# Optimization experiments

Hardware: AMD Instinct MI355X
Metric: run time of the kernel (lower is better)

Reference implementation:

```python
import jax, jax.numpy as jnp
import numpy as np

B, S, H = 32768, 16, 16  # batch, seq_len, G_hiddensize (code requires H == S and H == latent_dim == 16)
LATENT = 16
DISC_DIMS = [(1, 32), (32, 16), (16, 8), (8, 16), (16, 32)]


def setup_inputs() -> dict:
    key = jax.random.key(0)
    ks = iter(jax.random.split(key, 64))
    def p(shape, scale=0.1):
        return (jax.random.normal(next(ks), shape, dtype=jnp.float32) * scale)
    inp = dict(
        values=jax.random.normal(next(ks), (B, S), dtype=jnp.float32),
        masks=jax.random.randint(next(ks), (B, S), 0, 2).astype(jnp.int32),
        g_fwd_Wih=p((4 * H, 1)), g_fwd_Whh=p((4 * H, H)), g_fwd_b=p((4 * H,)),
        g_bwd_Wih=p((4 * H, 1)), g_bwd_Whh=p((4 * H, H)), g_bwd_b=p((4 * H,)),
        imp_W=p((1, H)), imp_b=p((1,)),
        fc_W=p((LATENT, H)), fc_b=p((LATENT,)),
        dec_Wih=p((4 * H, LATENT)), dec_Whh=p((4 * H, H)), dec_b=p((4 * H,)),
        dec_out_W=p((1, H)), dec_out_b=p((1,)),
        disc_out_W=p((1, 32)), disc_out_b=p((1,)),
    )
    for k, (i, h) in enumerate(DISC_DIMS):
        inp[f"d_W_{k}"] = p((4 * h, i))
        inp[f"d_b_{k}"] = p((4 * h,))
    return inp


def lstm_cell(x, h, c, Wih, Whh, b):
    gates = x @ Wih.T + h @ Whh.T + b
    i, f, g, o = jnp.split(gates, 4, axis=-1)
    c = jax.nn.sigmoid(f) * c + jax.nn.sigmoid(i) * jnp.tanh(g)
    h = jax.nn.sigmoid(o) * jnp.tanh(c)
    return h, c


def _forward(values, masks, g_fwd_Wih, g_fwd_Whh, g_fwd_b, g_bwd_Wih, g_bwd_Whh, g_bwd_b,
             imp_W, imp_b, fc_W, fc_b, dec_Wih, dec_Whh, dec_b, dec_out_W, dec_out_b,
             disc_out_W, disc_out_b,
             d_W_0, d_b_0, d_W_1, d_b_1, d_W_2, d_b_2, d_W_3, d_b_3, d_W_4, d_b_4):
    dt = values.dtype
    Bsz = values.shape[0]
    x = values[:, :, None]                     # (B, S, 1)
    m = masks.astype(dt)[:, :, None]           # (B, S, 1)
    # NOTE: torch.flip along axis 2 (size 1) is a no-op, so the bwd cell sees the
    # same (un-reversed) sequence as the fwd cell -- faithfully reproduced here.
    zH = jnp.zeros((Bsz, H), dt)
    h_f, c_f = lstm_cell(jnp.full((Bsz, 1), 128.0, dt), zH, zH, g_fwd_Wih, g_fwd_Whh, g_fwd_b)
    h_b, c_b = lstm_cell(jnp.full((Bsz, 1), -128.0, dt), zH, zH, g_bwd_Wih, g_bwd_Whh, g_bwd_b)

    def gen_step(carry, xm):
        h_f, c_f, h_b, c_b = carry
        x_t, m_t = xm                          # (B,1) each
        cc_f = (1 - m_t) * x_t + m_t * (h_f @ imp_W.T + imp_b)
        cc_b = (1 - m_t) * x_t + m_t * (h_b @ imp_W.T + imp_b)
        h_f, c_f = lstm_cell(cc_f, h_f, c_f, g_fwd_Wih, g_fwd_Whh, g_fwd_b)
        h_b, c_b = lstm_cell(cc_b, h_b, c_b, g_bwd_Wih, g_bwd_Whh, g_bwd_b)
        return (h_f, c_f, h_b, c_b), None

    (h_f, c_f, h_b, c_b), _ = jax.lax.scan(
        gen_step, (h_f, c_f, h_b, c_b),
        (jnp.transpose(x, (1, 0, 2)), jnp.transpose(m, (1, 0, 2))))
    h = h_f + h_b                               # (B, H), H == S
    imputations = h.reshape(Bsz, S, 1)
    imputed = imputations * (1 - m) + x * m      # (B, S, 1)

    # Discriminator: torch calls each LSTMCell WITHOUT state every timestep, so
    # hidden/cell start at zero each call -> purely feedforward per (batch, t).
    # W_hh @ 0 == 0, so only W_ih and the combined bias matter. Vectorize over B*S.
    inp = imputed.reshape(Bsz * S, 1)
    for W, b in ((d_W_0, d_b_0), (d_W_1, d_b_1), (d_W_2, d_b_2), (d_W_3, d_b_3), (d_W_4, d_b_4)):
        gates = inp @ W.T + b
        i, f, g, o = jnp.split(gates, 4, axis=-1)
        cc = jax.nn.sigmoid(i) * jnp.tanh(g)
        inp = jax.nn.sigmoid(o) * jnp.tanh(cc)
    disc_output = (inp @ disc_out_W.T + disc_out_b).reshape(Bsz, S, 1)

    latent = h @ fc_W.T + fc_b                  # (B, 16)

    # Decoder: ignores latent values (only uses batch size); start token = 128s.
    hd = cd = jnp.zeros((Bsz, H), dt)
    hd, cd = lstm_cell(jnp.full((Bsz, LATENT), 128.0, dt), hd, cd, dec_Wih, dec_Whh, dec_b)

    def dec_step(carry, _):
        hd, cd = carry
        hd, cd = lstm_cell(cd, hd, cd, dec_Wih, dec_Whh, dec_b)
        return (hd, cd), hd @ dec_out_W.T + dec_out_b

    _, outs = jax.lax.scan(dec_step, (hd, cd), None, length=S)  # (S, B, 1)
    reconstructed = jnp.transpose(outs, (1, 0, 2))
    return imputed, disc_output, latent, reconstructed


def reference(values, masks, g_fwd_Wih, g_fwd_Whh, g_fwd_b, g_bwd_Wih, g_bwd_Whh, g_bwd_b,
              imp_W, imp_b, fc_W, fc_b, dec_Wih, dec_Whh, dec_b, dec_out_W, dec_out_b,
              disc_out_W, disc_out_b,
              d_W_0, d_b_0, d_W_1, d_b_1, d_W_2, d_b_2, d_W_3, d_b_3, d_W_4, d_b_4):
    return _forward(values, masks, g_fwd_Wih, g_fwd_Whh, g_fwd_b, g_bwd_Wih, g_bwd_Whh, g_bwd_b,
                    imp_W, imp_b, fc_W, fc_b, dec_Wih, dec_Whh, dec_b, dec_out_W, dec_out_b,
                    disc_out_W, disc_out_b,
                    d_W_0, d_b_0, d_W_1, d_b_1, d_W_2, d_b_2, d_W_3, d_b_3, d_W_4, d_b_4)
```

## Files before the change

### kernel.cpp

```cpp
#include <hip/hip_runtime.h>

#define BB 32768
#define BS (BB*16)

typedef __attribute__((ext_vector_type(8))) short bf8v;
typedef __attribute__((ext_vector_type(4))) float f4v;

#define RECO 64
#define TAB  128
#define NTAB 2049
#define HFO  8448
#define HBO  (HFO+BS)

#define PW0 0
#define PB0 96
#define PW1 192
#define PB1 1920
#define PW2 1968
#define PB2 2448
#define PW3 2472
#define PB3 3048
#define PW4 3096
#define PB4 5016
#define POW 5112
#define POB 5144
#define PNU 5148

#define SMF 2580

#define NSCAN 1024
#define NTABB 129

__device__ __forceinline__ float sigm(float x){
    return __builtin_amdgcn_rcpf(1.f + __expf(-x));
}
__device__ __forceinline__ float tanh_f(float x){
    return 1.f - 2.f * __builtin_amdgcn_rcpf(1.f + __expf(2.f * x));
}
__device__ __forceinline__ float dunit(float gi, float gg, float go){
    return sigm(go) * tanh_f(sigm(gi) * tanh_f(gg));
}
__device__ __forceinline__ unsigned short f2bf(float f){
    union { float f; unsigned int i; } v; v.f = f;
    unsigned int x = v.i;
    unsigned int r = x + 0x7fffu + ((x >> 16) & 1u);
    return (unsigned short)(r >> 16);
}
__device__ __forceinline__ float bfu(unsigned short s){
    union { unsigned u; float f; } v; v.u = ((unsigned)s) << 16; return v.f;
}
__device__ __forceinline__ float bflo(unsigned p){
    union { unsigned u; float f; } v; v.u = p << 16; return v.f;
}
__device__ __forceinline__ float bfhi(unsigned p){
    union { unsigned u; float f; } v; v.u = p & 0xffff0000u; return v.f;
}

struct P29 { const float* p[29]; };

__device__ __forceinline__ bf8v makeB(const float* Whh, const float* Wih,
                                      int row, int quad)
{
    bf8v B = {0,0,0,0,0,0,0,0};
    if (quad < 2) {
        const float4* p = (const float4*)(Whh + row*16 + quad*8);
        float4 a0 = p[0], a1 = p[1];
        B[0]=(short)f2bf(a0.x); B[1]=(short)f2bf(a0.y);
        B[2]=(short)f2bf(a0.z); B[3]=(short)f2bf(a0.w);
        B[4]=(short)f2bf(a1.x); B[5]=(short)f2bf(a1.y);
        B[6]=(short)f2bf(a1.z); B[7]=(short)f2bf(a1.w);
    } else if (quad == 2) {
        B[0] = (short)f2bf(Wih[row]);
    }
    return B;
}

__global__ __launch_bounds__(256)
void k_main(P29 a, const int* __restrict__ masks, float* __restrict__ ws)
{
    __shared__ __align__(16) float smem[SMF];
    int tid = threadIdx.x;

    if (blockIdx.x >= NTABB + 1) {
        int lane = tid & 63;
        int wv   = tid >> 6;
        int m    = lane & 15;
        int quad = lane >> 4;
        int sb   = blockIdx.x - (NTABB + 1);
        int dir  = sb >= 512 ? 1 : 0;
        int gid0 = sb * 64 + wv * 16;
        int b0   = gid0 & 32767;

        const float* __restrict__ Wih = a.p[2 + 3*dir];
        const float* __restrict__ Whh = a.p[3 + 3*dir];
        const float* __restrict__ bia = a.p[4 + 3*dir];

        bf8v Ai = makeB(Whh, Wih, m,      quad);
        bf8v Af = makeB(Whh, Wih, 16+m,   quad);
        bf8v Ag = makeB(Whh, Wih, 32+m,   quad);
        bf8v Ao = makeB(Whh, Wih, 48+m,   quad);
        bf8v Ap = {0,0,0,0,0,0,0,0};
        if (quad < 2) {
            const float4* p = (const float4*)(a.p[8] + quad*8);
            float4 a0 = p[0], a1 = p[1];
            Ap[0]=(short)f2bf(a0.x); Ap[1]=(short)f2bf(a0.y);
            Ap[2]=(short)f2bf(a0.z); Ap[3]=(short)f2bf(a0.w);
            Ap[4]=(short)f2bf(a1.x); Ap[5]=(short)f2bf(a1.y);
            Ap[6]=(short)f2bf(a1.z); Ap[7]=(short)f2bf(a1.w);
        }
        float impb = a.p[9][0];
        f4v cimp = {impb, impb, impb, impb};

        f4v cbi, cbf, cbg, cbo;
        {
            float4 t;
            t = *(const float4*)(bia +      quad*4); cbi = (f4v){t.x,t.y,t.z,t.w};
            t = *(const float4*)(bia + 16 + quad*4); cbf = (f4v){t.x,t.y,t.z,t.w};
            t = *(const float4*)(bia + 32 + quad*4); cbg = (f4v){t.x,t.y,t.z,t.w};
            t = *(const float4*)(bia + 48 + quad*4); cbo = (f4v){t.x,t.y,t.z,t.w};
        }

        float sgn = dir ? -128.f : 128.f;
        float c[4], hl[4];
        {
            float4 wI = *(const float4*)(Wih +      quad*4);
            float4 wG = *(const float4*)(Wih + 32 + quad*4);
            float4 wO = *(const float4*)(Wih + 48 + quad*4);
            float wIv[4] = {wI.x, wI.y, wI.z, wI.w};
            float wGv[4] = {wG.x, wG.y, wG.z, wG.w};
            float wOv[4] = {wO.x, wO.y, wO.z, wO.w};
            #pragma unroll
            for (int r = 0; r < 4; r++) {
                float gi0 = sgn*wIv[r] + cbi[r];
                float gg0 = sgn*wGv[r] + cbg[r];
                float go0 = sgn*wOv[r] + cbo[r];
                float c0 = sigm(gi0) * tanh_f(gg0);
                c[r] = c0;
                hl[r] = sigm(go0) * tanh_f(c0);
            }
        }
        unsigned u01, u23;
        asm("v_cvt_pk_bf16_f32 %0, %1, %2" : "=v"(u01) : "v"(hl[0]), "v"(hl[1]));
        asm("v_cvt_pk_bf16_f32 %0, %1, %2" : "=v"(u23) : "v"(hl[2]), "v"(hl[3]));

        int pa0 = ((m + quad*32)      & 63) << 2;
        int pa1 = ((m + quad*32 + 16) & 63) << 2;

        const float* xrow = a.p[0] + (size_t)(b0 + m) * 16;
        const int*   mrow = masks  + (size_t)(b0 + m) * 16;

        #pragma unroll
        for (int t4 = 0; t4 < 4; t4++) {
            float4 x4 = *(const float4*)(xrow + t4*4);
            int4   m4 = *(const int4*)(mrow + t4*4);
            float xa[4] = {x4.x, x4.y, x4.z, x4.w};
            int   ma[4] = {m4.x, m4.y, m4.z, m4.w};
            #pragma unroll
            for (int j = 0; j < 4; j++) {
                union { int i[4]; bf8v v; } B;
                int w0 = __builtin_amdgcn_ds_bpermute(pa0, (int)u01);
                int w1 = __builtin_amdgcn_ds_bpermute(pa0, (int)u23);
                int w2 = __builtin_amdgcn_ds_bpermute(pa1, (int)u01);
                int w3 = __builtin_amdgcn_ds_bpermute(pa1, (int)u23);
                bool hi2 = quad >= 2;
                B.i[0] = hi2 ? 0 : w0;
                B.i[1] = hi2 ? 0 : w1;
                B.i[2] = hi2 ? 0 : w2;
                B.i[3] = hi2 ? 0 : w3;
                f4v dimp = __builtin_amdgcn_mfma_f32_16x16x32_bf16(Ap, B.v, cimp, 0, 0, 0);
                float cc = ma[j] ? dimp[0] : xa[j];
                unsigned ccw;
                asm("v_cvt_pk_bf16_f32 %0, %1, %2" : "=v"(ccw) : "v"(cc), "v"(0.f));
                B.i[0] = (quad == 2) ? (int)ccw : B.i[0];
                f4v di  = __builtin_amdgcn_mfma_f32_16x16x32_bf16(Ai, B.v, cbi, 0, 0, 0);
                f4v df_ = __builtin_amdgcn_mfma_f32_16x16x32_bf16(Af, B.v, cbf, 0, 0, 0);
                f4v dg  = __builtin_amdgcn_mfma_f32_16x16x32_bf16(Ag, B.v, cbg, 0, 0, 0);
                f4v dO  = __builtin_amdgcn_mfma_f32_16x16x32_bf16(Ao, B.v, cbo, 0, 0, 0);
                #pragma unroll
                for (int r = 0; r < 4; r++) {
                    float cn = sigm(df_[r]) * c[r] + sigm(di[r]) * tanh_f(dg[r]);
                    c[r] = cn;
                    hl[r] = sigm(dO[r]) * tanh_f(cn);
                }
                asm("v_cvt_pk_bf16_f32 %0, %1, %2" : "=v"(u01) : "v"(hl[0]), "v"(hl[1]));
                asm("v_cvt_pk_bf16_f32 %0, %1, %2" : "=v"(u23) : "v"(hl[2]), "v"(hl[3]));
            }
        }
        float* outp = ws + HFO + (size_t)dir*BS + (size_t)b0*16;
        #pragma unroll
        for (int r = 0; r < 4; r++) outp[m*16 + quad*4 + r] = hl[r];
        return;
    }

    if (blockIdx.x >= 1) {
        unsigned short* wl = (unsigned short*)smem;
#define STAGE(WS, BSi, h, K, padK, wdst, bdst) \
    { const float* Wp = a.p[WS]; const float* Bp2 = a.p[BSi]; \
      for (int i = tid; i < 3*(h)*(K); i += 256){ \
        int r = i/(K), k = i - r*(K); int g = r/(h), u0 = r - g*(h); \
        int sr = (g==0? u0 : (g==1? 2*(h)+u0 : 3*(h)+u0)); \
        wl[(wdst) + r*(padK) + k] = f2bf(Wp[sr*(K) + k]); } \
      for (int i = tid; i < 3*(h); i += 256){ \
        int g = i/(h), u0 = i - g*(h); \
        int sr = (g==0? u0 : (g==1? 2*(h)+u0 : 3*(h)+u0)); \
        wl[(bdst) + i] = f2bf(Bp2[sr]); } }
        STAGE(19, 20, 32,  1,  1, PW0, PB0)
        STAGE(21, 22, 16, 32, 36, PW1, PB1)
        STAGE(23, 24,  8, 16, 20, PW2, PB2)
        STAGE(25, 26, 16,  8, 12, PW3, PB3)
        STAGE(27, 28, 32, 16, 20, PW4, PB4)
#undef STAGE
        { const float* s = a.p[17]; for (int i = tid; i < 32; i += 256) wl[POW+i] = f2bf(s[i]); }
        if (tid == 0) wl[POB] = f2bf(a.p[18][0]);
        __syncthreads();
        int u = tid & 15;
        int gbase = (tid & 63) & 48;
        int gid = (blockIdx.x - 1) * 16 + (tid >> 4);
        const uint2* w2 = (const uint2*)wl;
        float xin = -8.f + (float)gid * (1.f/128.f);
        float lo = dunit(xin*bfu(wl[PW0+u])    + bfu(wl[PB0+u]),
                         xin*bfu(wl[PW0+32+u]) + bfu(wl[PB0+32+u]),
                         xin*bfu(wl[PW0+64+u]) + bfu(wl[PB0+64+u]));
        float hi = dunit(xin*bfu(wl[PW0+16+u]) + bfu(wl[PB0+16+u]),
                         xin*bfu(wl[PW0+48+u]) + bfu(wl[PB0+48+u]),
                         xin*bfu(wl[PW0+80+u]) + bfu(wl[PB0+80+u]));
        float A0[32];
        #pragma unroll
        for (int k = 0; k < 16; k++) { A0[k] = __shfl(lo, gbase+k); A0[16+k] = __shfl(hi, gbase+k); }
        float gi = bfu(wl[PB1+u]), gg = bfu(wl[PB1+16+u]), go = bfu(wl[PB1+32+u]);
        int bi_ = (PW1 + u*36)>>2, bg_ = (PW1 + (16+u)*36)>>2, bo_ = (PW1 + (32+u)*36)>>2;
        #pragma unroll
        for (int q = 0; q < 8; q++) {
            uint2 wi = w2[bi_+q], wg = w2[bg_+q], wo = w2[bo_+q];
            float b0=A0[4*q], b1=A0[4*q+1], b2=A0[4*q+2], b3=A0[4*q+3];
            gi += b0*bflo(wi.x) + b1*bfhi(wi.x) + b2*bflo(wi.y) + b3*bfhi(wi.y);
            gg += b0*bflo(wg.x) + b1*bfhi(wg.x) + b2*bflo(wg.y) + b3*bfhi(wg.y);
            go += b0*bflo(wo.x) + b1*bfhi(wo.x) + b2*bflo(wo.y) + b3*bfhi(wo.y);
        }
        float a1 = dunit(gi, gg, go);
        float A1[16];
        #pragma unroll
        for (int k = 0; k < 16; k++) A1[k] = __shfl(a1, gbase+k);
        int v = u & 7;
        gi = bfu(wl[PB2+v]); gg = bfu(wl[PB2+8+v]); go = bfu(wl[PB2+16+v]);
        bi_ = (PW2 + v*20)>>2; bg_ = (PW2 + (8+v)*20)>>2; bo_ = (PW2 + (16+v)*20)>>2;
        #pragma unroll
        for (int q = 0; q < 4; q++) {
            uint2 wi = w2[bi_+q], wg = w2[bg_+q], wo = w2[bo_+q];
            float b0=A1[4*q], b1=A1[4*q+1], b2=A1[4*q+2], b3=A1[4*q+3];
            gi += b0*bflo(wi.x) + b1*bfhi(wi.x) + b2*bflo(wi.y) + b3*bfhi(wi.y);
            gg += b0*bflo(wg.x) + b1*bfhi(wg.x) + b2*bflo(wg.y) + b3*bfhi(wg.y);
            go += b0*bflo(wo.x) + b1*bfhi(wo.x) + b2*bflo(wo.y) + b3*bfhi(wo.y);
        }
        float a2 = dunit(gi, gg, go);
        float A2[8];
        #pragma unroll
        for (int k = 0; k < 8; k++) A2[k] = __shfl(a2, gbase+k);
        gi = bfu(wl[PB3+u]); gg = bfu(wl[PB3+16+u]); go = bfu(wl[PB3+32+u]);
        bi_ = (PW3 + u*12)>>2; bg_ = (PW3 + (16+u)*12)>>2; bo_ = (PW3 + (32+u)*12)>>2;
        #pragma unroll
        for (int q = 0; q < 2; q++) {
            uint2 wi = w2[bi_+q], wg = w2[bg_+q], wo = w2[bo_+q];
            float b0=A2[4*q], b1=A2[4*q+1], b2=A2[4*q+2], b3=A2[4*q+3];
            gi += b0*bflo(wi.x) + b1*bfhi(wi.x) + b2*bflo(wi.y) + b3*bfhi(wi.y);
            gg += b0*bflo(wg.x) + b1*bfhi(wg.x) + b2*bflo(wg.y) + b3*bfhi(wg.y);
            go += b0*bflo(wo.x) + b1*bfhi(wo.x) + b2*bflo(wo.y) + b3*bfhi(wo.y);
        }
        float a3 = dunit(gi, gg, go);
        float A3[16];
        #pragma unroll
        for (int k = 0; k < 16; k++) A3[k] = __shfl(a3, gbase+k);
        float part;
        {
            float g0i = bfu(wl[PB4+u]),    g0g = bfu(wl[PB4+32+u]), g0o = bfu(wl[PB4+64+u]);
            float g1i = bfu(wl[PB4+16+u]), g1g = bfu(wl[PB4+48+u]), g1o = bfu(wl[PB4+80+u]);
            int c0i = (PW4 + u*20)>>2,      c0g = (PW4 + (32+u)*20)>>2, c0o = (PW4 + (64+u)*20)>>2;
            int c1i = (PW4 + (16+u)*20)>>2, c1g = (PW4 + (48+u)*20)>>2, c1o = (PW4 + (80+u)*20)>>2;
            #pragma unroll
            for (int q = 0; q < 4; q++) {
                float b0=A3[4*q], b1=A3[4*q+1], b2=A3[4*q+2], b3=A3[4*q+3];
                uint2 wi = w2[c0i+q], wg = w2[c0g+q], wo = w2[c0o+q];
                g0i += b0*bflo(wi.x) + b1*bfhi(wi.x) + b2*bflo(wi.y) + b3*bfhi(wi.y);
                g0g += b0*bflo(wg.x) + b1*bfhi(wg.x) + b2*bflo(wg.y) + b3*bfhi(wg.y);
                g0o += b0*bflo(wo.x) + b1*bfhi(wo.x) + b2*bflo(wo.y) + b3*bfhi(wo.y);
                wi = w2[c1i+q]; wg = w2[c1g+q]; wo = w2[c1o+q];
                g1i += b0*bflo(wi.x) + b1*bfhi(wi.x) + b2*bflo(wi.y) + b3*bfhi(wi.y);
                g1g += b0*bflo(wg.x) + b1*bfhi(wg.x) + b2*bflo(wg.y) + b3*bfhi(wg.y);
                g1o += b0*bflo(wo.x) + b1*bfhi(wo.x) + b2*bflo(wo.y) + b3*bfhi(wo.y);
            }
            part = dunit(g0i, g0g, g0o)*bfu(wl[POW+u]) + dunit(g1i, g1g, g1o)*bfu(wl[POW+16+u]);
        }
        part += __shfl_xor(part, 1);
        part += __shfl_xor(part, 2);
        part += __shfl_xor(part, 4);
        part += __shfl_xor(part, 8);
        if (u == 0 && gid < NTAB) ws[TAB + gid] = part + bfu(wl[POB]);
        return;
    }

    {
        float* dh = smem;
        float* dc = smem + 16;
        const float* Wih = a.p[12];
        const float* Whh = a.p[13];
        const float* bb  = a.p[14];
        const float* oW  = a.p[15];
        const float* ob  = a.p[16];
        float wii[16], wff[16], wgg[16], woo[16];
        float vii[16], vff[16], vgg[16], voo[16];
        float bi_r=0, bf_r=0, bg_r=0, bo_r=0;
        if (tid < 16) {
            int uu = tid;
            #pragma unroll
            for (int k = 0; k < 16; k++) {
                wii[k]=Wih[uu*16+k];      vii[k]=Whh[uu*16+k];
                wff[k]=Wih[(16+uu)*16+k]; vff[k]=Whh[(16+uu)*16+k];
                wgg[k]=Wih[(32+uu)*16+k]; vgg[k]=Whh[(32+uu)*16+k];
                woo[k]=Wih[(48+uu)*16+k]; voo[k]=Whh[(48+uu)*16+k];
            }
            bi_r=bb[uu]; bf_r=bb[16+uu]; bg_r=bb[32+uu]; bo_r=bb[48+uu];
            float gi = bi_r, gg = bg_r, go = bo_r;
            #pragma unroll
            for (int k = 0; k < 16; k++) {
                gi += 128.f * wii[k];
                gg += 128.f * wgg[k];
                go += 128.f * woo[k];
            }
            float cd0 = sigm(gi) * tanh_f(gg);
            dc[tid] = cd0; dh[tid] = sigm(go) * tanh_f(cd0);
        }
        __syncthreads();
        for (int t = 0; t < 16; t++) {
            float rx[16], rh[16], cold = 0.f;
            if (tid < 16) {
                #pragma unroll
                for (int k = 0; k < 16; k++) { rx[k] = dc[k]; rh[k] = dh[k]; }
                cold = dc[tid];
            }
            __syncthreads();
            if (tid < 16) {
                float gi = bi_r, gf = bf_r, gg = bg_r, go = bo_r;
                #pragma unroll
                for (int k = 0; k < 16; k++) {
                    gi += rx[k]*wii[k] + rh[k]*vii[k];
                    gf += rx[k]*wff[k] + rh[k]*vff[k];
                    gg += rx[k]*wgg[k] + rh[k]*vgg[k];
                    go += rx[k]*woo[k] + rh[k]*voo[k];
                }
                float cn = sigm(gf)*cold + sigm(gi)*tanh_f(gg);
                dc[tid] = cn; dh[tid] = sigm(go)*tanh_f(cn);
            }
            __syncthreads();
            if (tid == 0) {
                float o = ob[0];
                #pragma unroll
                for (int k = 0; k < 16; k++) o += dh[k] * oW[k];
                ws[RECO + t] = o;
            }
            __syncthreads();
        }
    }
}

__global__ __launch_bounds__(256) void k_post(P29 a, const int* __restrict__ masks,
                                              const float* __restrict__ ws,
                                              float* __restrict__ out)
{
    __shared__ float tab[NTAB];
    __shared__ __align__(16) float fw[256];
    __shared__ __align__(16) float rec[16];
    __shared__ float fb[16];
    int tid = threadIdx.x;
    for (int i = tid; i < NTAB; i += 256) tab[i] = ws[TAB + i];
    fw[tid] = a.p[10][tid];
    if (tid < 16) { fb[tid] = a.p[11][tid]; rec[tid] = ws[RECO + tid]; }
    __syncthreads();
    int T = blockIdx.x * 256 + tid;
    int b = T >> 2;
    int q = T & 3;
    int tq = q * 4;
    const float4* hf4 = (const float4*)(ws + HFO + (size_t)b*16);
    const float4* hb4 = (const float4*)(ws + HBO + (size_t)b*16);
    float4 s0, s1, s2, s3;
    {
        float4 f0=hf4[0], f1=hf4[1], f2=hf4[2], f3=hf4[3];
        float4 g0=hb4[0], g1=hb4[1], g2=hb4[2], g3=hb4[3];
        s0 = make_float4(f0.x+g0.x, f0.y+g0.y, f0.z+g0.z, f0.w+g0.w);
        s1 = make_float4(f1.x+g1.x, f1.y+g1.y, f1.z+g1.z, f1.w+g1.w);
        s2 = make_float4(f2.x+g2.x, f2.y+g2.y, f2.z+g2.z, f2.w+g2.w);
        s3 = make_float4(f3.x+g3.x, f3.y+g3.y, f3.z+g3.z, f3.w+g3.w);
    }
    float4 hq = (q==0) ? s0 : (q==1) ? s1 : (q==2) ? s2 : s3;
    float4 xv = *(const float4*)(a.p[0] + (size_t)b*16 + tq);
    int4   mv = *(const int4*)(masks + (size_t)b*16 + tq);
    float impv[4];
    impv[0] = mv.x ? xv.x : hq.x;
    impv[1] = mv.y ? xv.y : hq.y;
    impv[2] = mv.z ? xv.z : hq.z;
    impv[3] = mv.w ? xv.w : hq.w;
    float latv[4];
    #pragma unroll
    for (int j = 0; j < 4; j++) {
        int t = tq + j;
        const float4* wr = (const float4*)(fw + t*16);
        float4 w0=wr[0], w1=wr[1], w2=wr[2], w3=wr[3];
        float l = fb[t];
        l += s0.x*w0.x + s0.y*w0.y + s0.z*w0.z + s0.w*w0.w;
        l += s1.x*w1.x + s1.y*w1.y + s1.z*w1.z + s1.w*w1.w;
        l += s2.x*w2.x + s2.y*w2.y + s2.z*w2.z + s2.w*w2.w;
        l += s3.x*w3.x + s3.y*w3.y + s3.z*w3.z + s3.w*w3.w;
        latv[j] = l;
    }
    float dv[4];
    #pragma unroll
    for (int j = 0; j < 4; j++) {
        float xx = fminf(fmaxf(impv[j], -8.f), 8.f);
        float f = (xx + 8.f) * 128.f;
        float fi = floorf(f);
        int i = (int)fi; i = i > NTAB-2 ? NTAB-2 : i;
        float w = f - fi;
        dv[j] = fmaf(w, tab[i+1] - tab[i], tab[i]);
    }
    float4 rv = ((const float4*)rec)[q];
    size_t eo = (size_t)b*16 + tq;
    *(float4*)(out + eo)        = make_float4(impv[0], impv[1], impv[2], impv[3]);
    *(float4*)(out + BS + eo)   = make_float4(dv[0], dv[1], dv[2], dv[3]);
    *(float4*)(out + 2*BS + eo) = make_float4(latv[0], latv[1], latv[2], latv[3]);
    *(float4*)(out + 3*BS + eo) = rv;
}

extern "C" void kernel_launch(void* const* d_in, const int* in_sizes, int n_in,
                              void* d_out, int out_size, void* d_ws, size_t ws_size,
                              hipStream_t stream)
{
    float* ws = (float*)d_ws;
    P29 a;
    for (int i = 0; i < 29; i++) a.p[i] = (const float*)d_in[i];
    const int* masks = (const int*)d_in[1];
    k_main<<<1 + NTABB + NSCAN, 256, 0, stream>>>(a, masks, ws);
    k_post<<<(BB*4)/256, 256, 0, stream>>>(a, masks, ws, (float*)d_out);
}
```

Measured before the change: 154.0 us.

## Issue gate MFMAs before imputation and add x contribution in fp32; reorder blocks

The generator LSTM step no longer feeds the imputed input through the gate MFMAs, so all five MFMAs can issue together instead of waiting on the imputation MFMA result. The input-weight term is added afterwards with per-row fp32 FMAs, which also keeps that term out of bf16 precision. The scan blocks are moved to the lowest block indices so the long recurrent work is dispatched first, ahead of the table and reconstruction blocks. The cost is four extra FMAs per row per step and a few more registers for the input weights.

```diff
diff --git a/kernel.cpp b/kernel.cpp
--- a/kernel.cpp
+++ b/kernel.cpp
@@ -58,8 +58,7 @@
 
 struct P29 { const float* p[29]; };
 
-__device__ __forceinline__ bf8v makeB(const float* Whh, const float* Wih,
-                                      int row, int quad)
+__device__ __forceinline__ bf8v makeB(const float* Whh, int row, int quad)
 {
     bf8v B = {0,0,0,0,0,0,0,0};
     if (quad < 2) {
@@ -69,8 +68,6 @@
         B[2]=(short)f2bf(a0.z); B[3]=(short)f2bf(a0.w);
         B[4]=(short)f2bf(a1.x); B[5]=(short)f2bf(a1.y);
         B[6]=(short)f2bf(a1.z); B[7]=(short)f2bf(a1.w);
-    } else if (quad == 2) {
-        B[0] = (short)f2bf(Wih[row]);
     }
     return B;
 }
@@ -81,12 +78,12 @@
     __shared__ __align__(16) float smem[SMF];
     int tid = threadIdx.x;
 
-    if (blockIdx.x >= NTABB + 1) {
+    if (blockIdx.x < NSCAN) {
         int lane = tid & 63;
         int wv   = tid >> 6;
         int m    = lane & 15;
         int quad = lane >> 4;
-        int sb   = blockIdx.x - (NTABB + 1);
+        int sb   = blockIdx.x;
         int dir  = sb >= 512 ? 1 : 0;
         int gid0 = sb * 64 + wv * 16;
         int b0   = gid0 & 32767;
@@ -95,10 +92,10 @@
         const float* __restrict__ Whh = a.p[3 + 3*dir];
         const float* __restrict__ bia = a.p[4 + 3*dir];
 
-        bf8v Ai = makeB(Whh, Wih, m,      quad);
-        bf8v Af = makeB(Whh, Wih, 16+m,   quad);
-        bf8v Ag = makeB(Whh, Wih, 32+m,   quad);
-        bf8v Ao = makeB(Whh, Wih, 48+m,   quad);
+        bf8v Ai = makeB(Whh, m,      quad);
+        bf8v Af = makeB(Whh, 16+m,   quad);
+        bf8v Ag = makeB(Whh, 32+m,   quad);
+        bf8v Ao = makeB(Whh, 48+m,   quad);
         bf8v Ap = {0,0,0,0,0,0,0,0};
         if (quad < 2) {
             const float4* p = (const float4*)(a.p[8] + quad*8);
@@ -120,24 +117,28 @@
             t = *(const float4*)(bia + 48 + quad*4); cbo = (f4v){t.x,t.y,t.z,t.w};
         }
 
+        float wIv[4], wFv[4], wGv[4], wOv[4];
+        {
+            float4 wI = *(const float4*)(Wih +      quad*4);
+            float4 wF = *(const float4*)(Wih + 16 + quad*4);
+            float4 wG = *(const float4*)(Wih + 32 + quad*4);
+            float4 wO = *(const float4*)(Wih + 48 + quad*4);
+            wIv[0]=wI.x; wIv[1]=wI.y; wIv[2]=wI.z; wIv[3]=wI.w;
+            wFv[0]=wF.x; wFv[1]=wF.y; wFv[2]=wF.z; wFv[3]=wF.w;
+            wGv[0]=wG.x; wGv[1]=wG.y; wGv[2]=wG.z; wGv[3]=wG.w;
+            wOv[0]=wO.x; wOv[1]=wO.y; wOv[2]=wO.z; wOv[3]=wO.w;
+        }
+
         float sgn = dir ? -128.f : 128.f;
         float c[4], hl[4];
-        {
-            float4 wI = *(const float4*)(Wih +      quad*4);
-            float4 wG = *(const float4*)(Wih + 32 + quad*4);
-            float4 wO = *(const float4*)(Wih + 48 + quad*4);
-            float wIv[4] = {wI.x, wI.y, wI.z, wI.w};
-            float wGv[4] = {wG.x, wG.y, wG.z, wG.w};
-            float wOv[4] = {wO.x, wO.y, wO.z, wO.w};
-            #pragma unroll
-            for (int r = 0; r < 4; r++) {
-                float gi0 = sgn*wIv[r] + cbi[r];
-                float gg0 = sgn*wGv[r] + cbg[r];
-                float go0 = sgn*wOv[r] + cbo[r];
-                float c0 = sigm(gi0) * tanh_f(gg0);
-                c[r] = c0;
-                hl[r] = sigm(go0) * tanh_f(c0);
-            }
+        #pragma unroll
+        for (int r = 0; r < 4; r++) {
+            float gi0 = sgn*wIv[r] + cbi[r];
+            float gg0 = sgn*wGv[r] + cbg[r];
+            float go0 = sgn*wOv[r] + cbo[r];
+            float c0 = sigm(gi0) * tanh_f(gg0);
+            c[r] = c0;
+            hl[r] = sigm(go0) * tanh_f(c0);
         }
         unsigned u01, u23;
         asm("v_cvt_pk_bf16_f32 %0, %1, %2" : "=v"(u01) : "v"(hl[0]), "v"(hl[1]));
@@ -168,19 +169,20 @@
                 B.i[2] = hi2 ? 0 : w2;
                 B.i[3] = hi2 ? 0 : w3;
                 f4v dimp = __builtin_amdgcn_mfma_f32_16x16x32_bf16(Ap, B.v, cimp, 0, 0, 0);
+                f4v di   = __builtin_amdgcn_mfma_f32_16x16x32_bf16(Ai, B.v, cbi, 0, 0, 0);
+                f4v df_  = __builtin_amdgcn_mfma_f32_16x16x32_bf16(Af, B.v, cbf, 0, 0, 0);
+                f4v dg   = __builtin_amdgcn_mfma_f32_16x16x32_bf16(Ag, B.v, cbg, 0, 0, 0);
+                f4v dO   = __builtin_amdgcn_mfma_f32_16x16x32_bf16(Ao, B.v, cbo, 0, 0, 0);
                 float cc = ma[j] ? dimp[0] : xa[j];
-                unsigned ccw;
-                asm("v_cvt_pk_bf16_f32 %0, %1, %2" : "=v"(ccw) : "v"(cc), "v"(0.f));
-                B.i[0] = (quad == 2) ? (int)ccw : B.i[0];
-                f4v di  = __builtin_amdgcn_mfma_f32_16x16x32_bf16(Ai, B.v, cbi, 0, 0, 0);
-                f4v df_ = __builtin_amdgcn_mfma_f32_16x16x32_bf16(Af, B.v, cbf, 0, 0, 0);
-                f4v dg  = __builtin_amdgcn_mfma_f32_16x16x32_bf16(Ag, B.v, cbg, 0, 0, 0);
-                f4v dO  = __builtin_amdgcn_mfma_f32_16x16x32_bf16(Ao, B.v, cbo, 0, 0, 0);
                 #pragma unroll
                 for (int r = 0; r < 4; r++) {
-                    float cn = sigm(df_[r]) * c[r] + sigm(di[r]) * tanh_f(dg[r]);
+                    float gi = fmaf(wIv[r], cc, di[r]);
+                    float gf = fmaf(wFv[r], cc, df_[r]);
+                    float gg = fmaf(wGv[r], cc, dg[r]);
+                    float go = fmaf(wOv[r], cc, dO[r]);
+                    float cn = sigm(gf)*c[r] + sigm(gi)*tanh_f(gg);
                     c[r] = cn;
-                    hl[r] = sigm(dO[r]) * tanh_f(cn);
+                    hl[r] = sigm(go)*tanh_f(cn);
                 }
                 asm("v_cvt_pk_bf16_f32 %0, %1, %2" : "=v"(u01) : "v"(hl[0]), "v"(hl[1]));
                 asm("v_cvt_pk_bf16_f32 %0, %1, %2" : "=v"(u23) : "v"(hl[2]), "v"(hl[3]));
@@ -192,7 +194,7 @@
         return;
     }
 
-    if (blockIdx.x >= 1) {
+    if (blockIdx.x < NSCAN + NTABB) {
         unsigned short* wl = (unsigned short*)smem;
 #define STAGE(WS, BSi, h, K, padK, wdst, bdst) \
     { const float* Wp = a.p[WS]; const float* Bp2 = a.p[BSi]; \
@@ -215,7 +217,7 @@
         __syncthreads();
         int u = tid & 15;
         int gbase = (tid & 63) & 48;
-        int gid = (blockIdx.x - 1) * 16 + (tid >> 4);
+        int gid = (blockIdx.x - NSCAN) * 16 + (tid >> 4);
         const uint2* w2 = (const uint2*)wl;
         float xin = -8.f + (float)gid * (1.f/128.f);
         float lo = dunit(xin*bfu(wl[PW0+u])    + bfu(wl[PB0+u]),
@@ -437,6 +439,6 @@
     P29 a;
     for (int i = 0; i < 29; i++) a.p[i] = (const float*)d_in[i];
     const int* masks = (const int*)d_in[1];
-    k_main<<<1 + NTABB + NSCAN, 256, 0, stream>>>(a, masks, ws);
+    k_main<<<NSCAN + NTABB + 1, 256, 0, stream>>>(a, masks, ws);
     k_post<<<(BB*4)/256, 256, 0, stream>>>(a, masks, ws, (float*)d_out);
 }
```

Measured after the change: 154.6 us. Within noise of the previous version (+0.4%).

## Interleave two independent LSTM batch tiles per wave and reorder block roles

Applied to the files above, without the earlier changes.

Each wave in the recurrent scan now processes two independent 16-row batch tiles. Their bpermute, MFMA and activation chains are interleaved so one tile's latency can hide behind the other's, and the scan block count is halved. The scan blocks are moved to the front of the grid so the long recurrent work starts first, and launch bounds now request 3 blocks per CU. The cost is more live registers per thread and fewer waves available for parallelism.

```diff
diff --git a/kernel.cpp b/kernel.cpp
--- a/kernel.cpp
+++ b/kernel.cpp
@@ -28,7 +28,7 @@
 
 #define SMF 2580
 
-#define NSCAN 1024
+#define NSCAN 512
 #define NTABB 129
 
 __device__ __forceinline__ float sigm(float x){
@@ -75,21 +75,19 @@
     return B;
 }
 
-__global__ __launch_bounds__(256)
+__global__ __launch_bounds__(256, 3)
 void k_main(P29 a, const int* __restrict__ masks, float* __restrict__ ws)
 {
     __shared__ __align__(16) float smem[SMF];
     int tid = threadIdx.x;
 
-    if (blockIdx.x >= NTABB + 1) {
+    if (blockIdx.x < NSCAN) {
         int lane = tid & 63;
         int wv   = tid >> 6;
         int m    = lane & 15;
         int quad = lane >> 4;
-        int sb   = blockIdx.x - (NTABB + 1);
-        int dir  = sb >= 512 ? 1 : 0;
-        int gid0 = sb * 64 + wv * 16;
-        int b0   = gid0 & 32767;
+        int dir  = (int)(blockIdx.x >= 256);
+        int b0   = (blockIdx.x & 255) * 128 + wv * 32;
 
         const float* __restrict__ Wih = a.p[2 + 3*dir];
         const float* __restrict__ Whh = a.p[3 + 3*dir];
@@ -121,7 +119,7 @@
         }
 
         float sgn = dir ? -128.f : 128.f;
-        float c[4], hl[4];
+        float c[2][4], hl[2][4];
         {
             float4 wI = *(const float4*)(Wih +      quad*4);
             float4 wG = *(const float4*)(Wih + 32 + quad*4);
@@ -135,64 +133,83 @@
                 float gg0 = sgn*wGv[r] + cbg[r];
                 float go0 = sgn*wOv[r] + cbo[r];
                 float c0 = sigm(gi0) * tanh_f(gg0);
-                c[r] = c0;
-                hl[r] = sigm(go0) * tanh_f(c0);
-            }
-        }
-        unsigned u01, u23;
-        asm("v_cvt_pk_bf16_f32 %0, %1, %2" : "=v"(u01) : "v"(hl[0]), "v"(hl[1]));
-        asm("v_cvt_pk_bf16_f32 %0, %1, %2" : "=v"(u23) : "v"(hl[2]), "v"(hl[3]));
+                float h0 = sigm(go0) * tanh_f(c0);
+                c[0][r] = c0; c[1][r] = c0;
+                hl[0][r] = h0; hl[1][r] = h0;
+            }
+        }
+        unsigned u01[2], u23[2];
+        #pragma unroll
+        for (int s = 0; s < 2; s++) {
+            asm("v_cvt_pk_bf16_f32 %0, %1, %2" : "=v"(u01[s]) : "v"(hl[s][0]), "v"(hl[s][1]));
+            asm("v_cvt_pk_bf16_f32 %0, %1, %2" : "=v"(u23[s]) : "v"(hl[s][2]), "v"(hl[s][3]));
+        }
 
         int pa0 = ((m + quad*32)      & 63) << 2;
         int pa1 = ((m + quad*32 + 16) & 63) << 2;
 
-        const float* xrow = a.p[0] + (size_t)(b0 + m) * 16;
-        const int*   mrow = masks  + (size_t)(b0 + m) * 16;
+        const float* xrow0 = a.p[0] + (size_t)(b0 + m) * 16;
+        const int*   mrow0 = masks  + (size_t)(b0 + m) * 16;
+        const float* xrow1 = xrow0 + 16*16;
+        const int*   mrow1 = mrow0 + 16*16;
 
         #pragma unroll
         for (int t4 = 0; t4 < 4; t4++) {
-            float4 x4 = *(const float4*)(xrow + t4*4);
-            int4   m4 = *(const int4*)(mrow + t4*4);
-            float xa[4] = {x4.x, x4.y, x4.z, x4.w};
-            int   ma[4] = {m4.x, m4.y, m4.z, m4.w};
+            float4 xv0 = *(const float4*)(xrow0 + t4*4);
+            int4   mv0 = *(const int4*)(mrow0 + t4*4);
+            float4 xv1 = *(const float4*)(xrow1 + t4*4);
+            int4   mv1 = *(const int4*)(mrow1 + t4*4);
+            float xa[2][4] = {{xv0.x, xv0.y, xv0.z, xv0.w},
+                              {xv1.x, xv1.y, xv1.z, xv1.w}};
+            int   ma[2][4] = {{mv0.x, mv0.y, mv0.z, mv0.w},
+                              {mv1.x, mv1.y, mv1.z, mv1.w}};
             #pragma unroll
             for (int j = 0; j < 4; j++) {
-                union { int i[4]; bf8v v; } B;
-                int w0 = __builtin_amdgcn_ds_bpermute(pa0, (int)u01);
-                int w1 = __builtin_amdgcn_ds_bpermute(pa0, (int)u23);
-                int w2 = __builtin_amdgcn_ds_bpermute(pa1, (int)u01);
-                int w3 = __builtin_amdgcn_ds_bpermute(pa1, (int)u23);
-                bool hi2 = quad >= 2;
-                B.i[0] = hi2 ? 0 : w0;
-                B.i[1] = hi2 ? 0 : w1;
-                B.i[2] = hi2 ? 0 : w2;
-                B.i[3] = hi2 ? 0 : w3;
-                f4v dimp = __builtin_amdgcn_mfma_f32_16x16x32_bf16(Ap, B.v, cimp, 0, 0, 0);
-                float cc = ma[j] ? dimp[0] : xa[j];
-                unsigned ccw;
-                asm("v_cvt_pk_bf16_f32 %0, %1, %2" : "=v"(ccw) : "v"(cc), "v"(0.f));
-                B.i[0] = (quad == 2) ? (int)ccw : B.i[0];
-                f4v di  = __builtin_amdgcn_mfma_f32_16x16x32_bf16(Ai, B.v, cbi, 0, 0, 0);
-                f4v df_ = __builtin_amdgcn_mfma_f32_16x16x32_bf16(Af, B.v, cbf, 0, 0, 0);
-                f4v dg  = __builtin_amdgcn_mfma_f32_16x16x32_bf16(Ag, B.v, cbg, 0, 0, 0);
-                f4v dO  = __builtin_amdgcn_mfma_f32_16x16x32_bf16(Ao, B.v, cbo, 0, 0, 0);
+                union U4 { int i[4]; bf8v v; } B[2];
                 #pragma unroll
-                for (int r = 0; r < 4; r++) {
-                    float cn = sigm(df_[r]) * c[r] + sigm(di[r]) * tanh_f(dg[r]);
-                    c[r] = cn;
-                    hl[r] = sigm(dO[r]) * tanh_f(cn);
+                for (int s = 0; s < 2; s++) {
+                    int w0 = __builtin_amdgcn_ds_bpermute(pa0, (int)u01[s]);
+                    int w1 = __builtin_amdgcn_ds_bpermute(pa0, (int)u23[s]);
+                    int w2 = __builtin_amdgcn_ds_bpermute(pa1, (int)u01[s]);
+                    int w3 = __builtin_amdgcn_ds_bpermute(pa1, (int)u23[s]);
+                    bool hi2 = quad >= 2;
+                    B[s].i[0] = hi2 ? 0 : w0;
+                    B[s].i[1] = hi2 ? 0 : w1;
+                    B[s].i[2] = hi2 ? 0 : w2;
+                    B[s].i[3] = hi2 ? 0 : w3;
                 }
-                asm("v_cvt_pk_bf16_f32 %0, %1, %2" : "=v"(u01) : "v"(hl[0]), "v"(hl[1]));
-                asm("v_cvt_pk_bf16_f32 %0, %1, %2" : "=v"(u23) : "v"(hl[2]), "v"(hl[3]));
+                #pragma unroll
+                for (int s = 0; s < 2; s++) {
+                    f4v dimp = __builtin_amdgcn_mfma_f32_16x16x32_bf16(Ap, B[s].v, cimp, 0, 0, 0);
+                    float cc = ma[s][j] ? dimp[0] : xa[s][j];
+                    unsigned ccw;
+                    asm("v_cvt_pk_bf16_f32 %0, %1, %2" : "=v"(ccw) : "v"(cc), "v"(0.f));
+                    if (quad == 2) B[s].i[0] = (int)ccw;
+                    f4v di  = __builtin_amdgcn_mfma_f32_16x16x32_bf16(Ai, B[s].v, cbi, 0, 0, 0);
+                    f4v df_ = __builtin_amdgcn_mfma_f32_16x16x32_bf16(Af, B[s].v, cbf, 0, 0, 0);
+                    f4v dg  = __builtin_amdgcn_mfma_f32_16x16x32_bf16(Ag, B[s].v, cbg, 0, 0, 0);
+                    f4v dO  = __builtin_amdgcn_mfma_f32_16x16x32_bf16(Ao, B[s].v, cbo, 0, 0, 0);
+                    #pragma unroll
+                    for (int r = 0; r < 4; r++) {
+                        float cn = sigm(df_[r])*c[s][r] + sigm(di[r])*tanh_f(dg[r]);
+                        c[s][r] = cn;
+                        hl[s][r] = sigm(dO[r])*tanh_f(cn);
+                    }
+                    asm("v_cvt_pk_bf16_f32 %0, %1, %2" : "=v"(u01[s]) : "v"(hl[s][0]), "v"(hl[s][1]));
+                    asm("v_cvt_pk_bf16_f32 %0, %1, %2" : "=v"(u23[s]) : "v"(hl[s][2]), "v"(hl[s][3]));
+                }
             }
         }
         float* outp = ws + HFO + (size_t)dir*BS + (size_t)b0*16;
         #pragma unroll
-        for (int r = 0; r < 4; r++) outp[m*16 + quad*4 + r] = hl[r];
+        for (int r = 0; r < 4; r++) {
+            outp[m*16 + quad*4 + r]        = hl[0][r];
+            outp[(16 + m)*16 + quad*4 + r] = hl[1][r];
+        }
         return;
     }
 
-    if (blockIdx.x >= 1) {
+    if (blockIdx.x < NSCAN + NTABB) {
         unsigned short* wl = (unsigned short*)smem;
 #define STAGE(WS, BSi, h, K, padK, wdst, bdst) \
     { const float* Wp = a.p[WS]; const float* Bp2 = a.p[BSi]; \
@@ -215,7 +232,7 @@
         __syncthreads();
         int u = tid & 15;
         int gbase = (tid & 63) & 48;
-        int gid = (blockIdx.x - 1) * 16 + (tid >> 4);
+        int gid = (blockIdx.x - NSCAN) * 16 + (tid >> 4);
         const uint2* w2 = (const uint2*)wl;
         float xin = -8.f + (float)gid * (1.f/128.f);
         float lo = dunit(xin*bfu(wl[PW0+u])    + bfu(wl[PB0+u]),
@@ -437,6 +454,6 @@
     P29 a;
     for (int i = 0; i < 29; i++) a.p[i] = (const float*)d_in[i];
     const int* masks = (const int*)d_in[1];
-    k_main<<<1 + NTABB + NSCAN, 256, 0, stream>>>(a, masks, ws);
+    k_main<<<NSCAN + NTABB + 1, 256, 0, stream>>>(a, masks, ws);
     k_post<<<(BB*4)/256, 256, 0, stream>>>(a, masks, ws, (float*)d_out);
 }
```

Measured after the change: 154.8 us. Within noise of the previous version (+0.5%).
